# Optimization experiments

Measured on AMD Instinct MI355X. Metric: run time of the kernel, lower is better.

## Reference

```python
import jax, jax.numpy as jnp
import numpy as np
import math

B, C, MAPS, HEADS, F, W = 2, 8, 4, 8, 256, 1024
HD = F // HEADS  # head dim = 32


def conv2d(x, w, b):
    # x [B,Ci,H,W], w [Co,Ci,3,3], SAME padding 1
    y = jax.lax.conv_general_dilated(x, w, (1, 1), [(1, 1), (1, 1)],
                                     dimension_numbers=('NCHW', 'OIHW', 'NCHW'))
    return y + b[None, :, None, None]


def mcl_feat(x, w):
    # MultichannelLinear feature transform: per-channel linear over feature dim
    # x [B,C,Fin,W], w [C,Fout,Fin] -> [B,C,Fout,W]
    return jnp.einsum('bcfw,cgf->bcgw', x, w)


def rope(x):
    # lucidrains-style rotary embedding over seq dim (-2); x [..., S, D]
    d = x.shape[-1]
    s = x.shape[-2]
    inv = 1.0 / (10000.0 ** (jnp.arange(0, d, 2, dtype=jnp.float32) / d))
    fr = jnp.arange(s, dtype=jnp.float32)[:, None] * inv[None, :]  # [S, D/2]
    cos = jnp.repeat(jnp.cos(fr), 2, axis=-1).astype(x.dtype)  # [S, D]
    sin = jnp.repeat(jnp.sin(fr), 2, axis=-1).astype(x.dtype)
    x2 = x.reshape(*x.shape[:-1], d // 2, 2)
    xr = jnp.stack((-x2[..., 1], x2[..., 0]), axis=-1).reshape(x.shape)
    return x * cos + xr * sin


def setup_inputs() -> dict:
    key = jax.random.key(0)
    ks = jax.random.split(key, 16)
    p = lambda k, shp, s=0.02: (jax.random.normal(k, shp, dtype=jnp.float32) * s)
    inp = {
        'x': jax.random.normal(ks[0], (B, C, F, W), dtype=jnp.float32),
        'prev_qk': jax.random.normal(ks[1], (B, MAPS, HEADS, W, W), dtype=jnp.float32),
        'wq_conv': p(ks[2], (MAPS, C, 3, 3)), 'bq_conv': jnp.zeros((MAPS,), jnp.float32),
        'wq_lin': p(ks[3], (MAPS, F, F)),
        'wk_conv': p(ks[4], (MAPS, C, 3, 3)), 'bk_conv': jnp.zeros((MAPS,), jnp.float32),
        'wk_lin': p(ks[5], (MAPS, F, F)),
        'wv_conv': p(ks[6], (MAPS, C, 3, 3)), 'bv_conv': jnp.zeros((MAPS,), jnp.float32),
        'wv_lin': p(ks[7], (MAPS, F, F)),
        'wo_pw': p(ks[8], (C + MAPS, F, F)),
        'wo_dw': p(ks[9], (C, C + MAPS)),
    }
    return inp


def reference(x, prev_qk, wq_conv, bq_conv, wq_lin, wk_conv, bk_conv, wk_lin,
              wv_conv, bv_conv, wv_lin, wo_pw, wo_dw):
    b, c, h, w = x.shape

    def proj(w_conv, b_conv, w_lin):
        y = mcl_feat(conv2d(x, w_conv, b_conv), w_lin)  # [B,M,F,W]
        # transpose(2,3) -> [B,M,W,F] -> split heads -> [B,M,Hd,W? ] permute
        y = y.transpose(0, 1, 3, 2).reshape(b, MAPS, w, HEADS, HD)
        return y.transpose(0, 1, 3, 2, 4)  # [B,M,Heads,W,HD]

    q = rope(proj(wq_conv, bq_conv, wq_lin))
    k = rope(proj(wk_conv, bk_conv, wk_lin))
    v = proj(wv_conv, bv_conv, wv_lin)

    # NOTE: scale is sqrt(h) = sqrt(feature/height dim), as in the original code
    qk = jnp.einsum('bmnqd,bmnkd->bmnqk', q, k) / math.sqrt(h)
    qk = qk + prev_qk
    a = jnp.einsum('bmnqk,bmnkd->bmnqd', jax.nn.softmax(qk, axis=-1), v)
    # [B,M,Heads,W,HD] -> [B,M,W,Heads*HD] -> [B,M,F,W]
    a = a.transpose(0, 1, 3, 2, 4).reshape(b, MAPS, w, -1).transpose(0, 1, 3, 2)

    cat = jnp.concatenate((x, a), axis=1)  # [B, C+M, F, W]
    out = jnp.einsum('bcfw,oc->bofw', mcl_feat(cat, wo_pw), wo_dw)  # o_proj
    return out, qk
```

## Files before the change

### kernel.cpp

```cpp
#include <hip/hip_runtime.h>
#include <hip/hip_bf16.h>
#include <stdint.h>


typedef __attribute__((ext_vector_type(8))) short s16x8;
typedef __attribute__((ext_vector_type(4))) float f32x4;

#define MFMA16(a, b, c) __builtin_amdgcn_mfma_f32_16x16x32_bf16((a), (b), (c), 0, 0, 0)

__device__ __forceinline__ short f2bf(float f) {
  unsigned u = __builtin_bit_cast(unsigned, f);
  u = (u + 0x7FFFu + ((u >> 16) & 1u)) >> 16;
  return (short)u;
}
__device__ __forceinline__ unsigned pack2(float a, float b) {
  return (unsigned)(unsigned short)f2bf(a) | ((unsigned)(unsigned short)f2bf(b) << 16);
}
__device__ __forceinline__ float bf2f(unsigned u) {
  return __builtin_bit_cast(float, u << 16);
}

__global__ __launch_bounds__(256) void k_prep(const float* wq, const float* wk,
                                              const float* wv, const float* wo,
                                              short* wlin, short* wob, float* ct, float* st) {
  int i = blockIdx.x * 256 + threadIdx.x;
  if (i < 262144) wlin[i] = f2bf(wq[i]);
  else if (i < 524288) wlin[i] = f2bf(wk[i - 262144]);
  else if (i < 786432) wlin[i] = f2bf(wv[i - 524288]);
  if (i < 786432) wob[i] = f2bf(wo[i]);
  if (i < 16384) {
    int w = i >> 4, j = i & 15;
    float inv = exp2f(-(float)j * (13.287712379549449f / 16.0f));
    float ang = (float)w * inv;
    ct[i] = cosf(ang);
    st[i] = sinf(ang);
  }
}

__device__ __forceinline__ void loadrow(float* r, const float* xc, int f, int w0) {
  if (f < 0 || f > 255) {
#pragma unroll
    for (int jj = 0; jj < 6; ++jj) r[jj] = 0.f;
    return;
  }
  const float* row = xc + f * 1024;
#pragma unroll
  for (int jj = 0; jj < 6; ++jj) {
    int wc = w0 - 1 + jj;
    r[jj] = (wc >= 0 && wc < 1024) ? row[wc] : 0.f;
  }
}

__global__ __launch_bounds__(256) void k_conv(const float* x, const float* wqc, const float* bq,
                                              const float* wkc, const float* bk,
                                              const float* wvc, const float* bv, short* y) {
  int blk = blockIdx.x;
  int m_ = blk >> 7;
  int b_ = (blk >> 6) & 1;
  int fs = blk & 63;
  int f0 = fs * 4;
  int w0 = threadIdx.x * 4;
  const float* xb = x + (size_t)b_ * 2097152;
  const float* wp_[3] = {wqc + m_ * 72, wkc + m_ * 72, wvc + m_ * 72};
  float bias_[3] = {bq[m_], bk[m_], bv[m_]};

  float acc[3][4][4];
#pragma unroll
  for (int p = 0; p < 3; ++p)
#pragma unroll
    for (int fi = 0; fi < 4; ++fi)
#pragma unroll
      for (int j = 0; j < 4; ++j) acc[p][fi][j] = bias_[p];

  for (int c = 0; c < 8; ++c) {
    const float* xc = xb + c * 262144;
    float w9[3][9];
#pragma unroll
    for (int p = 0; p < 3; ++p)
#pragma unroll
      for (int t = 0; t < 9; ++t) w9[p][t] = wp_[p][c * 9 + t];
    float rows[6][6];
#pragma unroll
    for (int ri = 0; ri < 6; ++ri) loadrow(rows[ri], xc, f0 - 1 + ri, w0);
#pragma unroll
    for (int fi = 0; fi < 4; ++fi) {
#pragma unroll
      for (int p = 0; p < 3; ++p) {
#pragma unroll
        for (int j = 0; j < 4; ++j) {
          float s = acc[p][fi][j];
          s += rows[fi][j] * w9[p][0] + rows[fi][j + 1] * w9[p][1] + rows[fi][j + 2] * w9[p][2];
          s += rows[fi + 1][j] * w9[p][3] + rows[fi + 1][j + 1] * w9[p][4] + rows[fi + 1][j + 2] * w9[p][5];
          s += rows[fi + 2][j] * w9[p][6] + rows[fi + 2][j + 1] * w9[p][7] + rows[fi + 2][j + 2] * w9[p][8];
          acc[p][fi][j] = s;
        }
      }
    }
  }
#pragma unroll
  for (int p = 0; p < 3; ++p) {
    int mat = p * 8 + b_ * 4 + m_;
    short* yp = y + (size_t)mat * 262144;
#pragma unroll
    for (int fi = 0; fi < 4; ++fi) {
      uint2 pk;
      pk.x = pack2(acc[p][fi][0], acc[p][fi][1]);
      pk.y = pack2(acc[p][fi][2], acc[p][fi][3]);
      *(uint2*)(yp + (f0 + fi) * 1024 + w0) = pk;
    }
  }
}

__global__ __launch_bounds__(256) void k_ty(const short* y, short* yT) {
  __shared__ short tile[64][66];
  int blk = blockIdx.x;
  int mat = blk >> 6;
  int t = blk & 63;
  int f0 = (t >> 4) * 64, w0 = (t & 15) * 64;
  int j = threadIdx.x & 63, i0 = threadIdx.x >> 6;
  const short* sp = y + (size_t)mat * 262144 + f0 * 1024 + w0;
#pragma unroll
  for (int k = 0; k < 16; ++k) {
    int i = i0 + k * 4;
    tile[j][i] = sp[i * 1024 + j];
  }
  __syncthreads();
  short* dp = yT + (size_t)mat * 262144 + w0 * 256 + f0;
#pragma unroll
  for (int k = 0; k < 16; ++k) {
    int i = i0 + k * 4;
    dp[i * 256 + j] = tile[i][j];
  }
}

__global__ __launch_bounds__(256) void k_tx(const float* x, short* xT) {
  __shared__ short tile[64][66];
  int blk = blockIdx.x;
  int mat = blk >> 6;
  int t = blk & 63;
  int f0 = (t >> 4) * 64, w0 = (t & 15) * 64;
  int j = threadIdx.x & 63, i0 = threadIdx.x >> 6;
  const float* sp = x + (size_t)mat * 262144 + f0 * 1024 + w0;
#pragma unroll
  for (int k = 0; k < 16; ++k) {
    int i = i0 + k * 4;
    tile[j][i] = f2bf(sp[i * 1024 + j]);
  }
  __syncthreads();
  short* dp = xT + (size_t)mat * 262144 + w0 * 256 + f0;
#pragma unroll
  for (int k = 0; k < 16; ++k) {
    int i = i0 + k * 4;
    dp[i * 256 + j] = tile[i][j];
  }
}

__global__ __launch_bounds__(256) void k_qkv(const short* wlin, const short* yT,
                                             const float* ct, const float* st,
                                             short* qws, short* kws, short* vws) {
  int blk = blockIdx.x;
  int pbm = blk >> 4, wt = blk & 15;
  int p = pbm >> 3, bm = pbm & 7;
  int m_ = bm & 3;
  int tid = threadIdx.x, wv = tid >> 6, l = tid & 63, lr = l & 15, lg = l >> 4;
  const short* wl = wlin + (p * 4 + m_) * 65536;
  const short* yp = yT + (size_t)pbm * 262144;
  int w0 = wt * 64;
  int G0 = wv * 64;
  f32x4 acc[4][4];
#pragma unroll
  for (int i = 0; i < 4; ++i)
#pragma unroll
    for (int j = 0; j < 4; ++j) acc[i][j] = (f32x4){0.f, 0.f, 0.f, 0.f};

  if (p < 2) {
    for (int kc = 0; kc < 256; kc += 32) {
      s16x8 A[4], Bf[4];
#pragma unroll
      for (int gs = 0; gs < 4; ++gs)
        A[gs] = *(const s16x8*)(wl + (G0 + gs * 16 + lr) * 256 + kc + lg * 8);
#pragma unroll
      for (int s = 0; s < 4; ++s)
        Bf[s] = *(const s16x8*)(yp + (w0 + s * 16 + lr) * 256 + kc + lg * 8);
#pragma unroll
      for (int gs = 0; gs < 4; ++gs)
#pragma unroll
        for (int s = 0; s < 4; ++s) acc[gs][s] = MFMA16(A[gs], Bf[s], acc[gs][s]);
    }
    short* dst = (p == 0) ? qws : kws;
    float scale = (p == 0) ? 0.0625f : 1.0f;
#pragma unroll
    for (int gs = 0; gs < 4; ++gs) {
      int g0v = G0 + gs * 16 + lg * 4;
      int h = g0v >> 5, d0 = g0v & 31;
      int i0 = d0 >> 1;
#pragma unroll
      for (int s = 0; s < 4; ++s) {
        int w = w0 + s * 16 + lr;
        float c0 = ct[w * 16 + i0], sn0 = st[w * 16 + i0];
        float c1 = ct[w * 16 + i0 + 1], sn1 = st[w * 16 + i0 + 1];
        f32x4 v = acc[gs][s];
        float e0 = (v[0] * c0 - v[1] * sn0) * scale;
        float e1 = (v[1] * c0 + v[0] * sn0) * scale;
        float e2 = (v[2] * c1 - v[3] * sn1) * scale;
        float e3 = (v[3] * c1 + v[2] * sn1) * scale;
        uint2 pk;
        pk.x = pack2(e0, e1);
        pk.y = pack2(e2, e3);
        *(uint2*)(dst + (((size_t)bm * 8 + h) * 1024 + w) * 32 + d0) = pk;
      }
    }
  } else {
    for (int kc = 0; kc < 256; kc += 32) {
      s16x8 A[4], Bf[4];
#pragma unroll
      for (int s = 0; s < 4; ++s)
        A[s] = *(const s16x8*)(yp + (w0 + s * 16 + lr) * 256 + kc + lg * 8);
#pragma unroll
      for (int gs = 0; gs < 4; ++gs)
        Bf[gs] = *(const s16x8*)(wl + (G0 + gs * 16 + lr) * 256 + kc + lg * 8);
#pragma unroll
      for (int s = 0; s < 4; ++s)
#pragma unroll
        for (int gs = 0; gs < 4; ++gs) acc[s][gs] = MFMA16(A[s], Bf[gs], acc[s][gs]);
    }
#pragma unroll
    for (int s = 0; s < 4; ++s) {
      int wb = w0 + s * 16 + lg * 4;
#pragma unroll
      for (int gs = 0; gs < 4; ++gs) {
        int g = G0 + gs * 16 + lr;
        f32x4 v = acc[s][gs];
        uint2 pk;
        pk.x = pack2(v[0], v[1]);
        pk.y = pack2(v[2], v[3]);
        *(uint2*)(vws + ((size_t)bm * 256 + g) * 1024 + wb) = pk;
      }
    }
  }
}

__global__ __launch_bounds__(256, 1) void k_attn(const short* qws, const short* kws,
                                                 const short* vws, const float* prev,
                                                 float* qko, short* aT) {
  __shared__ char smem[155648];
  int blk = blockIdx.x;
  int bmh = blk >> 4;
  int qg = blk & 15;
  int h = bmh & 7, bm = bmh >> 3;
  int tid = threadIdx.x;
  int wv = tid >> 6, l = tid & 63, lr = l & 15, lg = l >> 4;
  const short* kp = kws + (size_t)bmh * 32768;
  const short* vp = vws + ((size_t)bm * 256 + h * 32) * 1024;

  {
    int row4 = tid >> 2, c = tid & 3;
#pragma unroll
    for (int i = 0; i < 16; ++i) {
      int row = i * 64 + row4;
      s16x8 kv = *(const s16x8*)(kp + row * 32 + c * 8);
      *(s16x8*)(smem + row * 64 + ((c * 16) ^ ((row & 3) << 4))) = kv;
    }
    int g2 = tid >> 7, cb = (tid & 127) * 16;
#pragma unroll
    for (int i = 0; i < 16; ++i) {
      int g = i * 2 + g2;
      s16x8 vv = *(const s16x8*)(vp + g * 1024 + (cb >> 1));
      *(s16x8*)(smem + 65536 + g * 2048 + (cb ^ ((g & 7) << 4))) = vv;
    }
  }
  __syncthreads();

  int q0 = qg * 64 + wv * 16;
  const short* qp = qws + (size_t)bmh * 32768;
  s16x8 qf = *(const s16x8*)(qp + (q0 + lr) * 32 + lg * 8);
  char* Sb = smem + 131072 + wv * 4096;
  char* Pb = smem + 147456 + wv * 2048;
  const float* pvb = prev + (size_t)bmh * 1048576 + (size_t)q0 * 1024;
  float* qob = qko + (size_t)bmh * 1048576 + (size_t)q0 * 1024;
  int pcol = (l & 15) * 4;
  int pcolb = pcol * 4;
  f32x4 o0 = {0.f, 0.f, 0.f, 0.f}, o1 = {0.f, 0.f, 0.f, 0.f};
  f32x4 rs = {0.f, 0.f, 0.f, 0.f};
  const f32x4 z4 = {0.f, 0.f, 0.f, 0.f};

  auto attn_win = [&](int w, f32x4(&pr)[4]) {
    int k0 = w * 64;
#pragma unroll
    for (int s = 0; s < 4; ++s) {
      int krow = k0 + s * 16 + lr;
      s16x8 kf = *(const s16x8*)(smem + krow * 64 + ((lg * 16) ^ ((krow & 3) << 4)));
      f32x4 sx = MFMA16(kf, qf, z4);
      *(f32x4*)(Sb + lr * 256 + ((s * 64 + lg * 16) ^ ((lr & 7) << 4))) = sx;
    }
#pragma unroll
    for (int j = 0; j < 4; ++j) {
      int qr = j * 4 + lg;
      f32x4 sv = *(const f32x4*)(Sb + qr * 256 + (pcolb ^ ((qr & 7) << 4)));
      f32x4 v = sv + pr[j];
      __builtin_nontemporal_store(v, (f32x4*)(qob + (size_t)qr * 1024 + k0 + pcol));
      float e0 = __expf(v[0]), e1 = __expf(v[1]);
      float e2 = __expf(v[2]), e3 = __expf(v[3]);
      rs[j] += (e0 + e1) + (e2 + e3);
      uint2 pk;
      pk.x = pack2(e0, e1);
      pk.y = pack2(e2, e3);
      *(uint2*)(Pb + qr * 128 + (((l & 15) * 8) ^ ((qr & 7) << 4))) = pk;
    }
    if (w + 2 < 16) {
#pragma unroll
      for (int j = 0; j < 4; ++j)
        pr[j] = *(const f32x4*)(pvb + (size_t)(j * 4 + lg) * 1024 + (w + 2) * 64 + pcol);
    }
#pragma unroll
    for (int kc = 0; kc < 2; ++kc) {
      s16x8 pa = *(const s16x8*)(Pb + lr * 128 + ((kc * 64 + lg * 16) ^ ((lr & 7) << 4)));
      int kcb = (k0 + kc * 32 + lg * 8) * 2;
      s16x8 vf0 = *(const s16x8*)(smem + 65536 + lr * 2048 + (kcb ^ ((lr & 7) << 4)));
      o0 = MFMA16(pa, vf0, o0);
      s16x8 vf1 = *(const s16x8*)(smem + 65536 + (16 + lr) * 2048 + (kcb ^ ((lr & 7) << 4)));
      o1 = MFMA16(pa, vf1, o1);
    }
  };

  f32x4 pA[4], pB[4];
#pragma unroll
  for (int j = 0; j < 4; ++j)
    pA[j] = *(const f32x4*)(pvb + (size_t)(j * 4 + lg) * 1024 + 0 + pcol);
#pragma unroll
  for (int j = 0; j < 4; ++j)
    pB[j] = *(const f32x4*)(pvb + (size_t)(j * 4 + lg) * 1024 + 64 + pcol);

  for (int w = 0; w < 16; w += 2) {
    attn_win(w, pA);
    attn_win(w + 1, pB);
  }

#pragma unroll
  for (int j = 0; j < 4; ++j) {
    float s = rs[j];
    s += __shfl_xor(s, 1);
    s += __shfl_xor(s, 2);
    s += __shfl_xor(s, 4);
    s += __shfl_xor(s, 8);
    rs[j] = s;
  }
  if (lr == 0) {
#pragma unroll
    for (int j = 0; j < 4; ++j) *(float*)(Sb + (j * 4 + lg) * 4) = rs[j];
  }
  f32x4 sums = *(const f32x4*)(Sb + lg * 16);
  f32x4 inv = {1.f / sums[0], 1.f / sums[1], 1.f / sums[2], 1.f / sums[3]};
  o0 *= inv;
  o1 *= inv;
  short* ap = aT + (size_t)bm * 262144;
#pragma unroll
  for (int r = 0; r < 4; ++r) {
    int row = q0 + lg * 4 + r;
    ap[row * 256 + h * 32 + lr] = f2bf(o0[r]);
    ap[row * 256 + h * 32 + 16 + lr] = f2bf(o1[r]);
  }
}

__global__ __launch_bounds__(256) void k_zproj(const short* wopw, const short* xT,
                                               const short* aT, short* z) {
  int blk = blockIdx.x;
  int bc = blk >> 4, wt = blk & 15;
  int b_ = bc / 12, c_ = bc % 12;
  const short* src = (c_ < 8) ? (xT + ((size_t)b_ * 8 + c_) * 262144)
                              : (aT + ((size_t)b_ * 4 + (c_ - 8)) * 262144);
  const short* wl = wopw + c_ * 65536;
  int tid = threadIdx.x, wv = tid >> 6, l = tid & 63, lr = l & 15, lg = l >> 4;
  int w0 = wt * 64, G0 = wv * 64;
  f32x4 acc[4][4];
#pragma unroll
  for (int i = 0; i < 4; ++i)
#pragma unroll
    for (int j = 0; j < 4; ++j) acc[i][j] = (f32x4){0.f, 0.f, 0.f, 0.f};
  for (int kc = 0; kc < 256; kc += 32) {
    s16x8 A[4], Bf[4];
#pragma unroll
    for (int s = 0; s < 4; ++s)
      A[s] = *(const s16x8*)(src + (w0 + s * 16 + lr) * 256 + kc + lg * 8);
#pragma unroll
    for (int gs = 0; gs < 4; ++gs)
      Bf[gs] = *(const s16x8*)(wl + (G0 + gs * 16 + lr) * 256 + kc + lg * 8);
#pragma unroll
    for (int s = 0; s < 4; ++s)
#pragma unroll
      for (int gs = 0; gs < 4; ++gs) acc[s][gs] = MFMA16(A[s], Bf[gs], acc[s][gs]);
  }
  short* zp = z + (size_t)bc * 262144;
#pragma unroll
  for (int s = 0; s < 4; ++s) {
    int wb = w0 + s * 16 + lg * 4;
#pragma unroll
    for (int gs = 0; gs < 4; ++gs) {
      int g = G0 + gs * 16 + lr;
      f32x4 v = acc[s][gs];
      uint2 pk;
      pk.x = pack2(v[0], v[1]);
      pk.y = pack2(v[2], v[3]);
      *(uint2*)(zp + g * 1024 + wb) = pk;
    }
  }
}

__global__ __launch_bounds__(256) void k_dw(const short* z, const float* dw, float* out0) {
  __shared__ float wdw[96];
  if (threadIdx.x < 96) wdw[threadIdx.x] = dw[threadIdx.x];
  __syncthreads();
  int id = blockIdx.x * 256 + threadIdx.x;
  int w4 = id & 255, g = (id >> 8) & 255, b_ = id >> 16;
  const short* zb = z + ((size_t)b_ * 12) * 262144 + g * 1024 + w4 * 4;
  float zv[12][4];
#pragma unroll
  for (int c = 0; c < 12; ++c) {
    uint2 u = *(const uint2*)(zb + (size_t)c * 262144);
    zv[c][0] = bf2f(u.x & 0xffffu);
    zv[c][1] = bf2f(u.x >> 16);
    zv[c][2] = bf2f(u.y & 0xffffu);
    zv[c][3] = bf2f(u.y >> 16);
  }
  float* ob = out0 + ((size_t)b_ * 8) * 262144 + g * 1024 + w4 * 4;
#pragma unroll
  for (int o = 0; o < 8; ++o) {
    f32x4 s = {0.f, 0.f, 0.f, 0.f};
#pragma unroll
    for (int c = 0; c < 12; ++c) {
      float wc = wdw[o * 12 + c];
      s[0] += wc * zv[c][0];
      s[1] += wc * zv[c][1];
      s[2] += wc * zv[c][2];
      s[3] += wc * zv[c][3];
    }
    __builtin_nontemporal_store(s, (f32x4*)(ob + (size_t)o * 262144));
  }
}

extern "C" void kernel_launch(void* const* d_in, const int* in_sizes, int n_in,
                              void* d_out, int out_size, void* d_ws, size_t ws_size,
                              hipStream_t stream) {
  const float* x = (const float*)d_in[0];
  const float* prevqk = (const float*)d_in[1];
  const float* wq_conv = (const float*)d_in[2];
  const float* bq = (const float*)d_in[3];
  const float* wq_lin = (const float*)d_in[4];
  const float* wk_conv = (const float*)d_in[5];
  const float* bk = (const float*)d_in[6];
  const float* wk_lin = (const float*)d_in[7];
  const float* wv_conv = (const float*)d_in[8];
  const float* bv = (const float*)d_in[9];
  const float* wv_lin = (const float*)d_in[10];
  const float* wo_pw = (const float*)d_in[11];
  const float* wo_dw = (const float*)d_in[12];

  float* out0 = (float*)d_out;
  float* qkout = out0 + 4194304;

  char* ws = (char*)d_ws;
  short* wlin_b = (short*)ws;
  short* wopw_b = wlin_b + 786432;
  float* ct = (float*)(ws + 3145728);
  float* st = ct + 16384;
  short* y_b = (short*)(ws + 3276800);
  short* yT_b = y_b + 6291456;
  short* q_b = yT_b + 6291456;
  short* k_b = q_b + 2097152;
  short* v_b = k_b + 2097152;
  short* xT_b = v_b + 2097152;
  short* aT_b = xT_b + 4194304;
  short* z_b = (short*)(ws + 53608448);

  k_prep<<<3072, 256, 0, stream>>>(wq_lin, wk_lin, wv_lin, wo_pw, wlin_b, wopw_b, ct, st);
  k_conv<<<512, 256, 0, stream>>>(x, wq_conv, bq, wk_conv, bk, wv_conv, bv, y_b);
  k_ty<<<1536, 256, 0, stream>>>(y_b, yT_b);
  k_tx<<<1024, 256, 0, stream>>>(x, xT_b);
  k_qkv<<<384, 256, 0, stream>>>(wlin_b, yT_b, ct, st, q_b, k_b, v_b);
  k_attn<<<1024, 256, 0, stream>>>(q_b, k_b, v_b, prevqk, qkout, aT_b);
  k_zproj<<<384, 256, 0, stream>>>(wopw_b, xT_b, aT_b, z_b);
  k_dw<<<512, 256, 0, stream>>>(z_b, wo_dw, out0);
}
```

Measured before the change: 232.6 us.

## Fuse y and x transposes into GEMM kernels via LDS tiles

Result: faster. 220.6 us (-5.1%).

```diff
diff --git a/kernel.cpp b/kernel.cpp
--- a/kernel.cpp
+++ b/kernel.cpp
@@ -111,62 +111,32 @@
   }
 }
 
-__global__ __launch_bounds__(256) void k_ty(const short* y, short* yT) {
-  __shared__ short tile[64][66];
-  int blk = blockIdx.x;
-  int mat = blk >> 6;
-  int t = blk & 63;
-  int f0 = (t >> 4) * 64, w0 = (t & 15) * 64;
-  int j = threadIdx.x & 63, i0 = threadIdx.x >> 6;
-  const short* sp = y + (size_t)mat * 262144 + f0 * 1024 + w0;
-#pragma unroll
-  for (int k = 0; k < 16; ++k) {
-    int i = i0 + k * 4;
-    tile[j][i] = sp[i * 1024 + j];
-  }
-  __syncthreads();
-  short* dp = yT + (size_t)mat * 262144 + w0 * 256 + f0;
-#pragma unroll
-  for (int k = 0; k < 16; ++k) {
-    int i = i0 + k * 4;
-    dp[i * 256 + j] = tile[i][j];
-  }
-}
-
-__global__ __launch_bounds__(256) void k_tx(const float* x, short* xT) {
-  __shared__ short tile[64][66];
-  int blk = blockIdx.x;
-  int mat = blk >> 6;
-  int t = blk & 63;
-  int f0 = (t >> 4) * 64, w0 = (t & 15) * 64;
-  int j = threadIdx.x & 63, i0 = threadIdx.x >> 6;
-  const float* sp = x + (size_t)mat * 262144 + f0 * 1024 + w0;
-#pragma unroll
-  for (int k = 0; k < 16; ++k) {
-    int i = i0 + k * 4;
-    tile[j][i] = f2bf(sp[i * 1024 + j]);
-  }
-  __syncthreads();
-  short* dp = xT + (size_t)mat * 262144 + w0 * 256 + f0;
-#pragma unroll
-  for (int k = 0; k < 16; ++k) {
-    int i = i0 + k * 4;
-    dp[i * 256 + j] = tile[i][j];
-  }
-}
-
-__global__ __launch_bounds__(256) void k_qkv(const short* wlin, const short* yT,
+__global__ __launch_bounds__(256) void k_qkv(const short* wlin, const short* y,
                                              const float* ct, const float* st,
                                              short* qws, short* kws, short* vws) {
+  __shared__ short ytile[64][264];
   int blk = blockIdx.x;
   int pbm = blk >> 4, wt = blk & 15;
   int p = pbm >> 3, bm = pbm & 7;
   int m_ = bm & 3;
   int tid = threadIdx.x, wv = tid >> 6, l = tid & 63, lr = l & 15, lg = l >> 4;
   const short* wl = wlin + (p * 4 + m_) * 65536;
-  const short* yp = yT + (size_t)pbm * 262144;
+  const short* yp = y + (size_t)pbm * 262144;
   int w0 = wt * 64;
   int G0 = wv * 64;
+
+  {
+    int h2 = l >> 5, lih = l & 31;
+#pragma unroll
+    for (int i = 0; i < 32; ++i) {
+      int f = wv * 64 + i * 2 + h2;
+      unsigned u = *(const unsigned*)(yp + f * 1024 + w0 + lih * 2);
+      ytile[lih * 2][f] = (short)(u & 0xffffu);
+      ytile[lih * 2 + 1][f] = (short)(u >> 16);
+    }
+  }
+  __syncthreads();
+
   f32x4 acc[4][4];
 #pragma unroll
   for (int i = 0; i < 4; ++i)
@@ -181,7 +151,7 @@
         A[gs] = *(const s16x8*)(wl + (G0 + gs * 16 + lr) * 256 + kc + lg * 8);
 #pragma unroll
       for (int s = 0; s < 4; ++s)
-        Bf[s] = *(const s16x8*)(yp + (w0 + s * 16 + lr) * 256 + kc + lg * 8);
+        Bf[s] = *(const s16x8*)(&ytile[s * 16 + lr][kc + lg * 8]);
 #pragma unroll
       for (int gs = 0; gs < 4; ++gs)
 #pragma unroll
@@ -215,7 +185,7 @@
       s16x8 A[4], Bf[4];
 #pragma unroll
       for (int s = 0; s < 4; ++s)
-        A[s] = *(const s16x8*)(yp + (w0 + s * 16 + lr) * 256 + kc + lg * 8);
+        A[s] = *(const s16x8*)(&ytile[s * 16 + lr][kc + lg * 8]);
 #pragma unroll
       for (int gs = 0; gs < 4; ++gs)
         Bf[gs] = *(const s16x8*)(wl + (G0 + gs * 16 + lr) * 256 + kc + lg * 8);
@@ -298,7 +268,7 @@
       int qr = j * 4 + lg;
       f32x4 sv = *(const f32x4*)(Sb + qr * 256 + (pcolb ^ ((qr & 7) << 4)));
       f32x4 v = sv + pr[j];
-      __builtin_nontemporal_store(v, (f32x4*)(qob + (size_t)qr * 1024 + k0 + pcol));
+      *(f32x4*)(qob + (size_t)qr * 1024 + k0 + pcol) = v;
       float e0 = __expf(v[0]), e1 = __expf(v[1]);
       float e2 = __expf(v[2]), e3 = __expf(v[3]);
       rs[j] += (e0 + e1) + (e2 + e3);
@@ -362,16 +332,31 @@
   }
 }
 
-__global__ __launch_bounds__(256) void k_zproj(const short* wopw, const short* xT,
+__global__ __launch_bounds__(256) void k_zproj(const short* wopw, const float* x,
                                                const short* aT, short* z) {
+  __shared__ short xtile[64][264];
   int blk = blockIdx.x;
   int bc = blk >> 4, wt = blk & 15;
   int b_ = bc / 12, c_ = bc % 12;
-  const short* src = (c_ < 8) ? (xT + ((size_t)b_ * 8 + c_) * 262144)
-                              : (aT + ((size_t)b_ * 4 + (c_ - 8)) * 262144);
   const short* wl = wopw + c_ * 65536;
   int tid = threadIdx.x, wv = tid >> 6, l = tid & 63, lr = l & 15, lg = l >> 4;
   int w0 = wt * 64, G0 = wv * 64;
+  bool use_lds = (c_ < 8);
+  const short* asrc = aT + ((size_t)b_ * 4 + (c_ - 8)) * 262144;
+
+  if (use_lds) {
+    const float* xp = x + ((size_t)b_ * 8 + c_) * 262144;
+    int h2 = l >> 5, lih = l & 31;
+#pragma unroll
+    for (int i = 0; i < 32; ++i) {
+      int f = wv * 64 + i * 2 + h2;
+      uint2 u = *(const uint2*)(xp + f * 1024 + w0 + lih * 2);
+      xtile[lih * 2][f] = f2bf(__builtin_bit_cast(float, u.x));
+      xtile[lih * 2 + 1][f] = f2bf(__builtin_bit_cast(float, u.y));
+    }
+  }
+  __syncthreads();
+
   f32x4 acc[4][4];
 #pragma unroll
   for (int i = 0; i < 4; ++i)
@@ -381,7 +366,8 @@
     s16x8 A[4], Bf[4];
 #pragma unroll
     for (int s = 0; s < 4; ++s)
-      A[s] = *(const s16x8*)(src + (w0 + s * 16 + lr) * 256 + kc + lg * 8);
+      A[s] = use_lds ? *(const s16x8*)(&xtile[s * 16 + lr][kc + lg * 8])
+                     : *(const s16x8*)(asrc + (w0 + s * 16 + lr) * 256 + kc + lg * 8);
 #pragma unroll
     for (int gs = 0; gs < 4; ++gs)
       Bf[gs] = *(const s16x8*)(wl + (G0 + gs * 16 + lr) * 256 + kc + lg * 8);
@@ -434,7 +420,7 @@
       s[2] += wc * zv[c][2];
       s[3] += wc * zv[c][3];
     }
-    __builtin_nontemporal_store(s, (f32x4*)(ob + (size_t)o * 262144));
+    *(f32x4*)(ob + (size_t)o * 262144) = s;
   }
 }
 
@@ -464,20 +450,16 @@
   float* ct = (float*)(ws + 3145728);
   float* st = ct + 16384;
   short* y_b = (short*)(ws + 3276800);
-  short* yT_b = y_b + 6291456;
-  short* q_b = yT_b + 6291456;
+  short* q_b = y_b + 6291456;
   short* k_b = q_b + 2097152;
   short* v_b = k_b + 2097152;
-  short* xT_b = v_b + 2097152;
-  short* aT_b = xT_b + 4194304;
+  short* aT_b = v_b + 2097152;
   short* z_b = (short*)(ws + 53608448);
 
   k_prep<<<3072, 256, 0, stream>>>(wq_lin, wk_lin, wv_lin, wo_pw, wlin_b, wopw_b, ct, st);
   k_conv<<<512, 256, 0, stream>>>(x, wq_conv, bq, wk_conv, bk, wv_conv, bv, y_b);
-  k_ty<<<1536, 256, 0, stream>>>(y_b, yT_b);
-  k_tx<<<1024, 256, 0, stream>>>(x, xT_b);
-  k_qkv<<<384, 256, 0, stream>>>(wlin_b, yT_b, ct, st, q_b, k_b, v_b);
+  k_qkv<<<384, 256, 0, stream>>>(wlin_b, y_b, ct, st, q_b, k_b, v_b);
   k_attn<<<1024, 256, 0, stream>>>(q_b, k_b, v_b, prevqk, qkout, aT_b);
-  k_zproj<<<384, 256, 0, stream>>>(wopw_b, xT_b, aT_b, z_b);
+  k_zproj<<<384, 256, 0, stream>>>(wopw_b, x, aT_b, z_b);
   k_dw<<<512, 256, 0, stream>>>(z_b, wo_dw, out0);
 }
```
